# Optimization experiments

Measured on AMD Instinct MI355X. Metric: run time of the kernel, lower is better.

## Reference

```python
import jax, jax.numpy as jnp
import numpy as np

SIGMA = 1.0
SQRT2 = float(np.sqrt(2.0))


def setup_inputs() -> dict:
    key = jax.random.key(0)
    k1, k2 = jax.random.split(key)
    B, L = 128, 1024
    preds = jax.random.normal(k1, (B, L), dtype=jnp.float32)
    # integer relevance grades 0..4, stored as float as in the torch module
    target = jax.random.randint(k2, (B, L), 0, 5).astype(jnp.float32)
    return {"preds": preds, "target": target}


def reference(preds, target):
    B, L = preds.shape
    # pairwise diff [B, L, L]: diff[b,i,j] = preds[b,i] - preds[b,j]
    diff = preds[:, :, None] - preds[:, None, :]
    # Normal(0, sigma*sqrt(2)).cdf(diff) == ndtr(diff / (sigma*sqrt(2)))
    p = jax.scipy.special.ndtr(diff / (SIGMA * SQRT2))
    # zero the diagonal (i == j) before summing
    eye = jnp.eye(L, dtype=bool)
    p = jnp.where(eye[None, :, :], 0.0, p)
    expected_ranks = 1.0 + p.sum(axis=2)  # [B, L]

    gains = 2.0 ** target - 1.0
    discounts = jnp.log2(expected_ranks + 1.0)
    dcg = (gains / discounts).sum(axis=1)  # [B]

    ideal_target = jnp.sort(target, axis=1)[:, ::-1]  # descending
    ideal_gains = 2.0 ** ideal_target - 1.0
    ideal_discounts = jnp.log2(jnp.arange(1, L + 1, dtype=jnp.float32) + 1.0)
    idcg = (ideal_gains / ideal_discounts).sum(axis=1)  # [B]

    ndcg = dcg / (idcg + 1e-10)
    return -ndcg.mean()
```

## Files before the change

kernel.cpp:

```cpp
#include <hip/hip_runtime.h>

#define B 128
#define L 1024

#if __has_builtin(__builtin_amdgcn_exp2f)
#define EXP2(x) __builtin_amdgcn_exp2f(x)
#else
#define EXP2(x) __expf((x) * 0.6931471805599453f)
#endif

#define WS_ACC  2048
#define WS_GCTR 2049

#define K1 -1.6279072f
#define K2 -0.9299637f
#define K3 -0.1074808f

__device__ __forceinline__ float erf_term(float pi, float pj) {
    float d = pi - pj;
    float a = __builtin_fabsf(d);
    float t = __builtin_fmaf(K3, a, K2);
    float u = __builtin_fmaf(t, a, K1);
    float e = EXP2(a * u);
    return __builtin_copysignf(1.0f - e, d);
}

__global__ __launch_bounds__(256, 8) void pair_kernel(const float* __restrict__ preds,
                                                      const float* __restrict__ target,
                                                      float* __restrict__ ws) {
    __shared__ float sp[L];
    __shared__ float red[256];

    const int blk  = blockIdx.x;
    const int b    = blk >> 3;
    const int iseg = blk & 7;
    const int tid  = threadIdx.x;
    const int il   = tid & 127;
    const int jh   = tid >> 7;

    if (blk == 0 && tid == 0) {
        ws[WS_ACC] = 0.0f;
        ((int*)ws)[WS_GCTR] = 0;
    }

    const float* prow = preds + b * L;

    float4 v4 = reinterpret_cast<const float4*>(prow)[tid];
    v4.x *= 0.5f; v4.y *= 0.5f; v4.z *= 0.5f; v4.w *= 0.5f;
    reinterpret_cast<float4*>(sp)[tid] = v4;

    const int i = iseg * 128 + il;
    const float tgt = (tid < 128) ? target[b * L + i] : 0.0f;

    __syncthreads();

    const float pi = sp[i];
    const float* sj = &sp[jh * 512];

    float a0 = 0.f, a1 = 0.f, a2 = 0.f, a3 = 0.f,
          a4 = 0.f, a5 = 0.f, a6 = 0.f, a7 = 0.f;
    for (int j = 0; j < 512; j += 8) {
        float4 va = *reinterpret_cast<const float4*>(&sj[j]);
        float4 vb = *reinterpret_cast<const float4*>(&sj[j + 4]);
        a0 += erf_term(pi, va.x);
        a1 += erf_term(pi, va.y);
        a2 += erf_term(pi, va.z);
        a3 += erf_term(pi, va.w);
        a4 += erf_term(pi, vb.x);
        a5 += erf_term(pi, vb.y);
        a6 += erf_term(pi, vb.z);
        a7 += erf_term(pi, vb.w);
    }
    float E = ((a0 + a1) + (a2 + a3)) + ((a4 + a5) + (a6 + a7));

    red[tid] = E;
    __syncthreads();

    if (tid < 128) {
        float Es = red[tid] + red[tid + 128];
        float er1 = 513.5f + 0.5f * Es;
        float g = EXP2(tgt) - 1.0f;
        float contrib = g * __builtin_amdgcn_rcpf(__log2f(er1));
        #pragma unroll
        for (int off = 32; off > 0; off >>= 1)
            contrib += __shfl_down(contrib, off);
        if ((tid & 63) == 0)
            ws[blk * 2 + (tid >> 6)] = contrib;
    }
}

__global__ __launch_bounds__(256) void finish_kernel(const float* __restrict__ target,
                                                     float* __restrict__ ws,
                                                     float* __restrict__ out) {
    __shared__ unsigned long long cred[256];
    __shared__ float2 fred[256];

    const int b   = blockIdx.x;
    const int tid = threadIdx.x;
    const float* trow = target + b * L;

    unsigned long long cnt = 0ull;
    #pragma unroll
    for (int k = 0; k < 4; ++k) {
        float t = trow[tid + k * 256];
        cnt += ((unsigned long long)(t > 3.5f) << 48)
             + ((unsigned long long)(t > 2.5f) << 32)
             + ((unsigned long long)(t > 1.5f) << 16)
             + ((unsigned long long)(t > 0.5f));
    }
    cred[tid] = cnt;
    __syncthreads();
    #pragma unroll
    for (int s = 128; s > 0; s >>= 1) {
        if (tid < (unsigned)s) cred[tid] += cred[tid + s];
        __syncthreads();
    }
    unsigned long long tot = cred[0];
    const int n4 = (int)(tot >> 48) & 0xFFFF;
    const int n3 = (int)(tot >> 32) & 0xFFFF;
    const int n2 = (int)(tot >> 16) & 0xFFFF;
    const int n1 = (int)(tot)       & 0xFFFF;

    float idcg_p = 0.0f;
    #pragma unroll
    for (int k = 0; k < 4; ++k) {
        int pos = tid + 1 + k * 256;
        float gain = (pos <= n4) ? 15.0f : (pos <= n3) ? 7.0f :
                     (pos <= n2) ? 3.0f  : (pos <= n1) ? 1.0f : 0.0f;
        idcg_p += gain * __builtin_amdgcn_rcpf(__log2f((float)pos + 1.0f));
    }
    float dcg_p = (tid < 16) ? ws[b * 16 + tid] : 0.0f;
    fred[tid] = make_float2(idcg_p, dcg_p);
    __syncthreads();
    #pragma unroll
    for (int s = 128; s > 0; s >>= 1) {
        if (tid < (unsigned)s) {
            float2 x = fred[tid], y = fred[tid + s];
            fred[tid] = make_float2(x.x + y.x, x.y + y.y);
        }
        __syncthreads();
    }

    if (tid == 0) {
        float ndcg = fred[0].y / (fred[0].x + 1e-10f);
        atomicAdd(&ws[WS_ACC], ndcg);
        __threadfence();
        int old = atomicAdd((int*)ws + WS_GCTR, 1);
        if (old == B - 1) {
            float acc = atomicAdd(&ws[WS_ACC], 0.0f);
            out[0] = -acc * (1.0f / (float)B);
        }
    }
}

extern "C" void kernel_launch(void* const* d_in, const int* in_sizes, int n_in,
                              void* d_out, int out_size, void* d_ws, size_t ws_size,
                              hipStream_t stream) {
    const float* preds  = (const float*)d_in[0];
    const float* target = (const float*)d_in[1];
    float* out = (float*)d_out;
    float* ws  = (float*)d_ws;

    pair_kernel<<<B * 8, 256, 0, stream>>>(preds, target, ws);
    finish_kernel<<<B, 256, 0, stream>>>(target, ws, out);
}
```

Baseline: 90.34 us.

## Exploit pairwise antisymmetry to halve erf evaluations using DPP ring rotation

Each pairwise term is now computed once and credited to both endpoints, since the term for (j,i) is the negation of the term for (i,j). Groups of 16 lanes rotate partner values with DPP row rotates and accumulate the negated contributions for the partner side. Those contributions go into a shared-memory buffer through LDS atomics, and each block writes per-row partial sums to the workspace. The finish kernel then sums the partials and computes DCG. This roughly halves the transcendental work, at the cost of DPP rotates, LDS atomics, a larger workspace and more global traffic between the kernels.

Result: no change. 88.96 us (-1.5%).

```diff
diff --git a/kernel.cpp b/kernel.cpp
--- a/kernel.cpp
+++ b/kernel.cpp
@@ -9,34 +9,33 @@
 #define EXP2(x) __expf((x) * 0.6931471805599453f)
 #endif
 
-#define WS_ACC  2048
-#define WS_GCTR 2049
+#define WS_ACC  1048576
+#define WS_GCTR 1048577
 
 #define K1 -1.6279072f
 #define K2 -0.9299637f
 #define K3 -0.1074808f
 
-__device__ __forceinline__ float erf_term(float pi, float pj) {
-    float d = pi - pj;
-    float a = __builtin_fabsf(d);
-    float t = __builtin_fmaf(K3, a, K2);
-    float u = __builtin_fmaf(t, a, K1);
-    float e = EXP2(a * u);
-    return __builtin_copysignf(1.0f - e, d);
+__device__ __forceinline__ float ror16(float x) {
+    int i = __float_as_int(x);
+    i = __builtin_amdgcn_update_dpp(i, i, 0x121 , 0xF, 0xF, true);
+    return __int_as_float(i);
 }
 
 __global__ __launch_bounds__(256, 8) void pair_kernel(const float* __restrict__ preds,
-                                                      const float* __restrict__ target,
                                                       float* __restrict__ ws) {
     __shared__ float sp[L];
-    __shared__ float red[256];
+    __shared__ float ebuf[L];
 
     const int blk  = blockIdx.x;
     const int b    = blk >> 3;
-    const int iseg = blk & 7;
+    const int hb   = blk & 7;
     const int tid  = threadIdx.x;
-    const int il   = tid & 127;
-    const int jh   = tid >> 7;
+    const int l16  = tid & 15;
+    const int ring = tid >> 4;
+    const int slot = hb * 16 + ring;
+    const int g    = slot & 63;
+    const int half = slot >> 6;
 
     if (blk == 0 && tid == 0) {
         ws[WS_ACC] = 0.0f;
@@ -44,49 +43,41 @@
     }
 
     const float* prow = preds + b * L;
-
-    float4 v4 = reinterpret_cast<const float4*>(prow)[tid];
-    v4.x *= 0.5f; v4.y *= 0.5f; v4.z *= 0.5f; v4.w *= 0.5f;
-    reinterpret_cast<float4*>(sp)[tid] = v4;
-
-    const int i = iseg * 128 + il;
-    const float tgt = (tid < 128) ? target[b * L + i] : 0.0f;
-
+    float4 v = reinterpret_cast<const float4*>(prow)[tid];
+    v.x *= 0.5f; v.y *= 0.5f; v.z *= 0.5f; v.w *= 0.5f;
+    reinterpret_cast<float4*>(sp)[tid] = v;
+    reinterpret_cast<float4*>(ebuf)[tid] = make_float4(0.f, 0.f, 0.f, 0.f);
     __syncthreads();
 
-    const float pi = sp[i];
-    const float* sj = &sp[jh * 512];
+    const float pi = sp[g * 16 + l16];
+    float Ei = 0.0f;
 
-    float a0 = 0.f, a1 = 0.f, a2 = 0.f, a3 = 0.f,
-          a4 = 0.f, a5 = 0.f, a6 = 0.f, a7 = 0.f;
-    for (int j = 0; j < 512; j += 8) {
-        float4 va = *reinterpret_cast<const float4*>(&sj[j]);
-        float4 vb = *reinterpret_cast<const float4*>(&sj[j + 4]);
-        a0 += erf_term(pi, va.x);
-        a1 += erf_term(pi, va.y);
-        a2 += erf_term(pi, va.z);
-        a3 += erf_term(pi, va.w);
-        a4 += erf_term(pi, vb.x);
-        a5 += erf_term(pi, vb.y);
-        a6 += erf_term(pi, vb.z);
-        a7 += erf_term(pi, vb.w);
+    const int nt = half ? (16 + (g < 32 ? 1 : 0)) : 16;
+    for (int si = 0; si < nt; ++si) {
+        const int s  = half ? (16 + si) : si;
+        const int gj = (g + s) & 63;
+        float pj = sp[gj * 16 + l16];
+        float ej = 0.0f;
+        #pragma unroll
+        for (int k = 0; k < 16; ++k) {
+            pj = ror16(pj);
+            float d = pi - pj;
+            float a = __builtin_fabsf(d);
+            float t = __builtin_fmaf(K3, a, K2);
+            float u = __builtin_fmaf(t, a, K1);
+            float e = EXP2(a * u);
+            float r = __builtin_copysignf(1.0f - e, d);
+            Ei += r;
+            ej = ror16(ej) - r;
+        }
+        if (s != 0)
+            atomicAdd(&ebuf[gj * 16 + l16], ej);
     }
-    float E = ((a0 + a1) + (a2 + a3)) + ((a4 + a5) + (a6 + a7));
-
-    red[tid] = E;
+    atomicAdd(&ebuf[g * 16 + l16], Ei);
     __syncthreads();
 
-    if (tid < 128) {
-        float Es = red[tid] + red[tid + 128];
-        float er1 = 513.5f + 0.5f * Es;
-        float g = EXP2(tgt) - 1.0f;
-        float contrib = g * __builtin_amdgcn_rcpf(__log2f(er1));
-        #pragma unroll
-        for (int off = 32; off > 0; off >>= 1)
-            contrib += __shfl_down(contrib, off);
-        if ((tid & 63) == 0)
-            ws[blk * 2 + (tid >> 6)] = contrib;
-    }
+    float4 r4 = reinterpret_cast<float4*>(ebuf)[tid];
+    reinterpret_cast<float4*>(ws + (size_t)blk * L)[tid] = r4;
 }
 
 __global__ __launch_bounds__(256) void finish_kernel(const float* __restrict__ target,
@@ -99,10 +90,18 @@
     const int tid = threadIdx.x;
     const float* trow = target + b * L;
 
+    float dcg_p = 0.0f;
     unsigned long long cnt = 0ull;
     #pragma unroll
     for (int k = 0; k < 4; ++k) {
-        float t = trow[tid + k * 256];
+        const int i = tid + k * 256;
+        float E = 0.0f;
+        #pragma unroll
+        for (int hb = 0; hb < 8; ++hb)
+            E += ws[(size_t)(b * 8 + hb) * L + i];
+        float er1 = 513.5f + 0.5f * E;
+        float t = trow[i];
+        dcg_p += (EXP2(t) - 1.0f) * __builtin_amdgcn_rcpf(__log2f(er1));
         cnt += ((unsigned long long)(t > 3.5f) << 48)
              + ((unsigned long long)(t > 2.5f) << 32)
              + ((unsigned long long)(t > 1.5f) << 16)
@@ -115,7 +114,7 @@
         if (tid < (unsigned)s) cred[tid] += cred[tid + s];
         __syncthreads();
     }
-    unsigned long long tot = cred[0];
+    const unsigned long long tot = cred[0];
     const int n4 = (int)(tot >> 48) & 0xFFFF;
     const int n3 = (int)(tot >> 32) & 0xFFFF;
     const int n2 = (int)(tot >> 16) & 0xFFFF;
@@ -129,7 +128,6 @@
                      (pos <= n2) ? 3.0f  : (pos <= n1) ? 1.0f : 0.0f;
         idcg_p += gain * __builtin_amdgcn_rcpf(__log2f((float)pos + 1.0f));
     }
-    float dcg_p = (tid < 16) ? ws[b * 16 + tid] : 0.0f;
     fred[tid] = make_float2(idcg_p, dcg_p);
     __syncthreads();
     #pragma unroll
@@ -161,6 +159,6 @@
     float* out = (float*)d_out;
     float* ws  = (float*)d_ws;
 
-    pair_kernel<<<B * 8, 256, 0, stream>>>(preds, target, ws);
+    pair_kernel<<<B * 8, 256, 0, stream>>>(preds, ws);
     finish_kernel<<<B, 256, 0, stream>>>(target, ws, out);
 }
```

## Compute pairwise erf terms in packed fp16 with windowed half accumulators

Applied to the files above, without the earlier changes.

Stores the half-scaled predictions in shared memory as fp16 and evaluates the erf polynomial with packed half2 arithmetic, so each instruction handles two pairs. Partial sums stay in half2 over 64-element windows and are then flushed to an fp32 total, which limits accumulation error. The exp2 step still runs per half lane. This reduces ALU and LDS traffic per pair, at the cost of fp16 rounding in both the differences and the partial sums, which may hurt accuracy.

Result: no change. 88.57 us (-2.0%).

```diff
diff --git a/kernel.cpp b/kernel.cpp
--- a/kernel.cpp
+++ b/kernel.cpp
@@ -1,4 +1,5 @@
 #include <hip/hip_runtime.h>
+#include <hip/hip_fp16.h>
 
 #define B 128
 #define L 1024
@@ -9,26 +10,36 @@
 #define EXP2(x) __expf((x) * 0.6931471805599453f)
 #endif
 
+typedef unsigned int uint4v __attribute__((ext_vector_type(4)));
+
 #define WS_ACC  2048
 #define WS_GCTR 2049
 
-#define K1 -1.6279072f
-#define K2 -0.9299637f
-#define K3 -0.1074808f
+#define K1f -1.6279072f
+#define K2f -0.9299637f
+#define K3f -0.1074808f
 
-__device__ __forceinline__ float erf_term(float pi, float pj) {
-    float d = pi - pj;
-    float a = __builtin_fabsf(d);
-    float t = __builtin_fmaf(K3, a, K2);
-    float u = __builtin_fmaf(t, a, K1);
-    float e = EXP2(a * u);
-    return __builtin_copysignf(1.0f - e, d);
+__device__ __forceinline__ void term2(unsigned int du, __half2 pi2,
+                                      __half2 k1, __half2 k2, __half2 k3,
+                                      __half2 one2, __half2& acc) {
+    __half2 pj = __builtin_bit_cast(__half2, du);
+    __half2 d  = __hsub2(pi2, pj);
+    unsigned int dbits = __builtin_bit_cast(unsigned int, d);
+    __half2 a  = __builtin_bit_cast(__half2, dbits & 0x7fff7fffu);
+    __half2 t  = __hfma2(k3, a, k2);
+    __half2 u  = __hfma2(t,  a, k1);
+    __half2 w  = __hmul2(a, u);
+    __half2 e  = __halves2half2(hexp2(__low2half(w)),
+                                hexp2(__high2half(w)));
+    __half2 r  = __hsub2(one2, e);
+    unsigned int rb = __builtin_bit_cast(unsigned int, r) | (dbits & 0x80008000u);
+    acc = __hadd2(acc, __builtin_bit_cast(__half2, rb));
 }
 
 __global__ __launch_bounds__(256, 8) void pair_kernel(const float* __restrict__ preds,
                                                       const float* __restrict__ target,
                                                       float* __restrict__ ws) {
-    __shared__ float sp[L];
+    __shared__ __align__(16) __half sph[L];
     __shared__ float red[256];
 
     const int blk  = blockIdx.x;
@@ -46,32 +57,42 @@
     const float* prow = preds + b * L;
 
     float4 v4 = reinterpret_cast<const float4*>(prow)[tid];
-    v4.x *= 0.5f; v4.y *= 0.5f; v4.z *= 0.5f; v4.w *= 0.5f;
-    reinterpret_cast<float4*>(sp)[tid] = v4;
+    __half2 h01 = __floats2half2_rn(0.5f * v4.x, 0.5f * v4.y);
+    __half2 h23 = __floats2half2_rn(0.5f * v4.z, 0.5f * v4.w);
+    reinterpret_cast<__half2*>(sph)[tid * 2 + 0] = h01;
+    reinterpret_cast<__half2*>(sph)[tid * 2 + 1] = h23;
 
     const int i = iseg * 128 + il;
     const float tgt = (tid < 128) ? target[b * L + i] : 0.0f;
 
     __syncthreads();
 
-    const float pi = sp[i];
-    const float* sj = &sp[jh * 512];
+    const __half2 pi2  = __half2half2(sph[i]);
+    const __half2 k1   = __floats2half2_rn(K1f, K1f);
+    const __half2 k2   = __floats2half2_rn(K2f, K2f);
+    const __half2 k3   = __floats2half2_rn(K3f, K3f);
+    const __half2 one2 = __floats2half2_rn(1.0f, 1.0f);
+    const __half2 z2   = __floats2half2_rn(0.0f, 0.0f);
 
-    float a0 = 0.f, a1 = 0.f, a2 = 0.f, a3 = 0.f,
-          a4 = 0.f, a5 = 0.f, a6 = 0.f, a7 = 0.f;
-    for (int j = 0; j < 512; j += 8) {
-        float4 va = *reinterpret_cast<const float4*>(&sj[j]);
-        float4 vb = *reinterpret_cast<const float4*>(&sj[j + 4]);
-        a0 += erf_term(pi, va.x);
-        a1 += erf_term(pi, va.y);
-        a2 += erf_term(pi, va.z);
-        a3 += erf_term(pi, va.w);
-        a4 += erf_term(pi, vb.x);
-        a5 += erf_term(pi, vb.y);
-        a6 += erf_term(pi, vb.z);
-        a7 += erf_term(pi, vb.w);
+    const uint4v* basep = reinterpret_cast<const uint4v*>(sph + jh * 512);
+
+    float E = 0.0f;
+    for (int wdw = 0; wdw < 8; ++wdw) {
+        __half2 A0 = z2, A1 = z2, A2 = z2, A3 = z2;
+        #pragma unroll
+        for (int m = 0; m < 8; ++m) {
+            uint4v q = basep[wdw * 8 + m];
+            term2(q.x, pi2, k1, k2, k3, one2, A0);
+            term2(q.y, pi2, k1, k2, k3, one2, A1);
+            term2(q.z, pi2, k1, k2, k3, one2, A2);
+            term2(q.w, pi2, k1, k2, k3, one2, A3);
+        }
+        float2 f0 = __half22float2(A0);
+        float2 f1 = __half22float2(A1);
+        float2 f2 = __half22float2(A2);
+        float2 f3 = __half22float2(A3);
+        E += ((f0.x + f0.y) + (f1.x + f1.y)) + ((f2.x + f2.y) + (f3.x + f3.y));
     }
-    float E = ((a0 + a1) + (a2 + a3)) + ((a4 + a5) + (a6 + a7));
 
     red[tid] = E;
     __syncthreads();
```
